# Performance work log

Measured on AMD Instinct MI355X. Metric: run time of the kernel, lower is better.

The kernel has to match this reference:

```python
import jax, jax.numpy as jnp
import numpy as np

MIN_SIZE = 16.0
PH, PW, SCALE = 7, 7, 0.0625


def _context_anchor(rois, hh, hw):
    """rois: [N,5] (batch_idx,x1,y1,x2,y2). Returns [N*8,5] context boxes, col0 = 0 label."""
    N = rois.shape[0]
    x1, y1, x2, y2 = rois[:, 1], rois[:, 2], rois[:, 3], rois[:, 4]
    w, h = x2 - x1, y2 - y1
    k = jnp.arange(3, dtype=rois.dtype)
    sx = x1[:, None] + w[:, None] * (k - 0.5)  # x1 - w + w*k + w/2
    sy = y1[:, None] + h[:, None] * (k - 0.5)
    # np.meshgrid(shift_x, shift_y).ravel() is y-major
    cx = jnp.broadcast_to(sx[:, None, :], (N, 3, 3)).reshape(N, 9)
    cy = jnp.broadcast_to(sy[:, :, None], (N, 3, 3)).reshape(N, 9)
    boxes = jnp.stack([cx - w[:, None] / 4, cy - h[:, None] / 4,
                       cx + w[:, None] / 4, cy + h[:, None] / 4], -1)  # [N,9,4]
    bw = boxes[..., 2] - boxes[..., 0] + 1
    bh = boxes[..., 3] - boxes[..., 1] + 1
    invalid = ((boxes[..., 0] < 0) | (boxes[..., 1] < 0) |
               (boxes[..., 2] >= hw) | (boxes[..., 3] >= hh) |
               (bw < MIN_SIZE) | (bh < MIN_SIZE))
    boxes = jnp.where(invalid[..., None], rois[:, None, 1:5], boxes)
    boxes = boxes[:, jnp.array([0, 1, 2, 3, 5, 6, 7, 8]), :]  # drop center cell
    gt = boxes.reshape(N * 8, 4)  # K = 8N
    # IoU(all roi boxes, gt) with +1 pixel convention (bbox_overlaps_batch)
    A = rois[:, 1:5]
    aw, ah = A[:, 2] - A[:, 0] + 1, A[:, 3] - A[:, 1] + 1
    gw, gh = gt[:, 2] - gt[:, 0] + 1, gt[:, 3] - gt[:, 1] + 1
    iw = jnp.maximum(jnp.minimum(A[:, None, 2], gt[None, :, 2]) - jnp.maximum(A[:, None, 0], gt[None, :, 0]) + 1, 0)
    ih = jnp.maximum(jnp.minimum(A[:, None, 3], gt[None, :, 3]) - jnp.maximum(A[:, None, 1], gt[None, :, 1]) + 1, 0)
    inter = iw * ih
    ov = inter / ((aw * ah)[:, None] + (gw * gh)[None, :] - inter)  # [N,K]
    ov = jnp.where(((gw == 1) & (gh == 1))[None, :], 0.0, ov)
    ov = jnp.where(((aw == 1) & (ah == 1))[:, None], -1.0, ov)
    gt_max = ov.max(0)          # best overlap per gt box
    best = ov.argmax(0)         # index of best-matching roi (torch's `_`)
    labels = gt_max >= 0.3
    w_cell, h_cell = gt[:, 2] - gt[:, 0], gt[:, 3] - gt[:, 1]
    rw = jnp.where(labels, rois[best, 3] - rois[best, 1], 0.0)
    rh = jnp.where(labels, rois[best, 4] - rois[best, 2], 0.0)
    labels = (labels & ~(jnp.maximum(rw, rh) >= jnp.maximum(w_cell, h_cell))
                     & ~(jnp.minimum(rw, rh) < jnp.minimum(w_cell, h_cell) / 3))
    gt = jnp.where(labels[:, None], rois[best][:, 1:5], gt)
    # original zeroes labels at the end -> label column is all zeros
    return jnp.concatenate([jnp.zeros((N * 8, 1), rois.dtype), gt], -1)


def _roi_pool(features, boxes, ph, pw, scale):
    """Classic Caffe max RoIPool. Assumes batch_size==1 (all batch indices 0)."""
    _, C, H, W = features.shape
    f = features[0]  # [C,H,W]
    sw = jnp.round(boxes[:, 1] * scale)
    sh = jnp.round(boxes[:, 2] * scale)
    ew = jnp.round(boxes[:, 3] * scale)
    eh = jnp.round(boxes[:, 4] * scale)
    bsh = jnp.maximum(eh - sh + 1, 1.0) / ph
    bsw = jnp.maximum(ew - sw + 1, 1.0) / pw
    ii = jnp.arange(ph, dtype=f.dtype)
    jj = jnp.arange(pw, dtype=f.dtype)
    hs = jnp.clip(jnp.floor(ii[None, :] * bsh[:, None]) + sh[:, None], 0, H)   # [R,ph]
    he = jnp.clip(jnp.ceil((ii[None, :] + 1) * bsh[:, None]) + sh[:, None], 0, H)
    ws = jnp.clip(jnp.floor(jj[None, :] * bsw[:, None]) + sw[:, None], 0, W)   # [R,pw]
    we = jnp.clip(jnp.ceil((jj[None, :] + 1) * bsw[:, None]) + sw[:, None], 0, W)
    hidx = jnp.arange(H, dtype=f.dtype)
    widx = jnp.arange(W, dtype=f.dtype)
    mask_h = (hidx >= hs[..., None]) & (hidx < he[..., None])  # [R,ph,H]
    mask_w = (widx >= ws[..., None]) & (widx < we[..., None])  # [R,pw,W]
    NEG = jnp.asarray(-1e30, f.dtype)
    # separable masked max: reduce W per pw-bin, then H per ph-bin
    colmax = jnp.stack([jnp.where(mask_w[:, j, None, None, :], f[None], NEG).max(-1)
                        for j in range(pw)], axis=1)           # [R,pw,C,H]
    out = jnp.stack([jnp.where(mask_h[:, i, None, None, :], colmax, NEG).max(-1)
                     for i in range(ph)], axis=1)              # [R,ph,pw,C]
    valid = mask_h.any(-1)[:, :, None] & mask_w.any(-1)[:, None, :]
    out = jnp.where(valid[..., None], out, 0.0)                # empty bins -> 0
    return jnp.transpose(out, (0, 3, 1, 2))                    # [R,C,ph,pw]


def reference(features, rois, hh, hw):
    N = rois.shape[0]
    gt = _context_anchor(rois, hh, hw).reshape(N, 8, 5)
    cat_rois = jnp.concatenate([rois[:, None, :], gt], 1).reshape(-1, 5)  # [9N,5]
    pool = _roi_pool(features, cat_rois, PH, PW, SCALE)                   # [9N,C,7,7]
    pool_feat = pool.reshape(N, -1, PW, PH)                               # [N,9C,7,7]
    return pool_feat, cat_rois


def setup_inputs() -> dict:
    key = jax.random.key(0)
    k1, k2, k3, k4, k5 = jax.random.split(key, 5)
    N, C, Hf, Wf, IMG = 32, 256, 40, 40, 640
    x1 = jax.random.uniform(k1, (N,), minval=0.0, maxval=IMG - 220.0)
    y1 = jax.random.uniform(k2, (N,), minval=0.0, maxval=IMG - 220.0)
    bw = jax.random.uniform(k3, (N,), minval=80.0, maxval=200.0)
    bh = jax.random.uniform(k4, (N,), minval=80.0, maxval=200.0)
    rois = jnp.stack([jnp.zeros((N,)), x1, y1, x1 + bw, y1 + bh], -1).astype(jnp.float32)
    features = jax.random.normal(k5, (1, C, Hf, Wf), dtype=jnp.float32)
    return {"features": features, "rois": rois, "hh": 640, "hw": 640}
```

## Files before the change

### kernel.cpp

```cpp
#include <hip/hip_runtime.h>
#include <math.h>

#define N_ROIS   32
#define N_CAT    (N_ROIS * 9)
#define C_FEAT   256
#define H_FEAT   40
#define W_FEAT   40
#define P_FEAT   (H_FEAT * W_FEAT)
#define PH       7
#define PW       7
#define SCALE    0.0625f
#define MIN_SIZE 16.0f
#define CELLS    (PH * PW)
#define POOL_PER_BOX (C_FEAT * CELLS)
#define OUT_POOL_ELEMS ((size_t)N_CAT * POOL_PER_BOX)

#define CH_G     64
#define NCHG     4
#define NBLK     (N_CAT * NCHG)
#define TPB      448
#define WROWS    14
#define WCOLS    14
#define XSTRIDE  65
#define YSTRIDE  (WROWS * XSTRIDE)
#define WIN_FLTS (WROWS * YSTRIDE + 220)

__global__ __launch_bounds__(TPB) void
fused_v6(const float* __restrict__ f,
         const float* __restrict__ rois,
         const int* __restrict__ hh_p,
         const int* __restrict__ hw_p,
         float* __restrict__ out) {
    __shared__ __align__(16) float win[WIN_FLTS];

    const int bid  = blockIdx.x;
    const int s    = (bid & 7) * (NBLK / 8) + (bid >> 3);
    const int b    = s >> 2;
    const int cg   = s & 3;
    const int tid  = threadIdx.x;
    const int lane = tid & 63;

    const int n  = b / 9;
    const int jj = b % 9;
    const float x1 = rois[n * 5 + 1], y1 = rois[n * 5 + 2];
    const float x2 = rois[n * 5 + 3], y2 = rois[n * 5 + 4];
    float bx1, by1, bx2, by2;

    if (jj == 0) {
        bx1 = x1; by1 = y1; bx2 = x2; by2 = y2;
    } else {
        const int j = jj - 1;
        const int m = (j < 4) ? j : j + 1;
        const int r  = m / 3;
        const int cc = m % 3;
        const float w = x2 - x1, h = y2 - y1;
        const float cx = x1 + w * ((float)cc - 0.5f);
        const float cy = y1 + h * ((float)r  - 0.5f);
        bx1 = cx - w * 0.25f;
        by1 = cy - h * 0.25f;
        bx2 = cx + w * 0.25f;
        by2 = cy + h * 0.25f;
        const float bw = bx2 - bx1 + 1.0f;
        const float bh = by2 - by1 + 1.0f;
        const float hh = (float)(*hh_p);
        const float hw = (float)(*hw_p);
        const bool invalid = (bx1 < 0.0f) || (by1 < 0.0f) ||
                             (bx2 >= hw) || (by2 >= hh) ||
                             (bw < MIN_SIZE) || (bh < MIN_SIZE);
        if (invalid) { bx1 = x1; by1 = y1; bx2 = x2; by2 = y2; }

        const float gw = bx2 - bx1 + 1.0f;
        const float gh = by2 - by1 + 1.0f;
        const float garea = gw * gh;
        const bool gdeg = (gw == 1.0f) && (gh == 1.0f);

        const int a = lane & 31;
        const float ax1 = rois[a * 5 + 1], ay1 = rois[a * 5 + 2];
        const float ax2 = rois[a * 5 + 3], ay2 = rois[a * 5 + 4];
        const float aw = ax2 - ax1 + 1.0f, ah = ay2 - ay1 + 1.0f;
        const float iw = fmaxf(fminf(ax2, bx2) - fmaxf(ax1, bx1) + 1.0f, 0.0f);
        const float ih = fmaxf(fminf(ay2, by2) - fmaxf(ay1, by1) + 1.0f, 0.0f);
        const float inter = iw * ih;
        float ov = inter / (aw * ah + garea - inter);
        if (gdeg) ov = 0.0f;
        if (aw == 1.0f && ah == 1.0f) ov = -1.0f;
        int ai = a;
        #pragma unroll
        for (int off = 32; off >= 1; off >>= 1) {
            const float o2 = __shfl_xor(ov, off);
            const int   a2 = __shfl_xor(ai, off);
            if (o2 > ov || (o2 == ov && a2 < ai)) { ov = o2; ai = a2; }
        }

        bool label = (ov >= 0.3f);
        const float w_cell = bx2 - bx1;
        const float h_cell = by2 - by1;
        const float rw = label ? (rois[ai * 5 + 3] - rois[ai * 5 + 1]) : 0.0f;
        const float rh = label ? (rois[ai * 5 + 4] - rois[ai * 5 + 2]) : 0.0f;
        label = label &&
                !(fmaxf(rw, rh) >= fmaxf(w_cell, h_cell)) &&
                !(fminf(rw, rh) < fminf(w_cell, h_cell) / 3.0f);
        if (label) {
            bx1 = rois[ai * 5 + 1]; by1 = rois[ai * 5 + 2];
            bx2 = rois[ai * 5 + 3]; by2 = rois[ai * 5 + 4];
        }
    }

    if (cg == 0 && tid == 0) {
        float* row = out + OUT_POOL_ELEMS + (size_t)b * 5;
        row[0] = (jj == 0) ? rois[n * 5] : 0.0f;
        row[1] = bx1; row[2] = by1; row[3] = bx2; row[4] = by2;
    }

    const float sw = rintf(bx1 * SCALE);
    const float sh = rintf(by1 * SCALE);
    const float ew = rintf(bx2 * SCALE);
    const float eh = rintf(by2 * SCALE);
    const float bsh = fmaxf(eh - sh + 1.0f, 1.0f) * (1.0f / (float)PH);
    const float bsw = fmaxf(ew - sw + 1.0f, 1.0f) * (1.0f / (float)PW);

    const int cl = tid & 63;
    const int i  = tid >> 6;

    const int hs = __builtin_amdgcn_readfirstlane(
        (int)fminf(fmaxf(floorf((float)i * bsh) + sh, 0.0f), (float)H_FEAT));
    const int he = __builtin_amdgcn_readfirstlane(
        (int)fminf(fmaxf(ceilf((float)(i + 1) * bsh) + sh, 0.0f), (float)H_FEAT));

    int ws[PW], we[PW];
    #pragma unroll
    for (int j = 0; j < PW; ++j) {
        ws[j] = __builtin_amdgcn_readfirstlane(
            (int)fminf(fmaxf(floorf((float)j * bsw) + sw, 0.0f), (float)W_FEAT));
        we[j] = __builtin_amdgcn_readfirstlane(
            (int)fminf(fmaxf(ceilf((float)(j + 1) * bsw) + sw, 0.0f), (float)W_FEAT));
    }
    const int xs = ws[0];
    const int ys = __builtin_amdgcn_readfirstlane(
        (int)fminf(fmaxf(sh, 0.0f), (float)H_FEAT));

    const bool narrow = (bsw <= 2.0f) && (bsh <= 2.0f);

    float mx[PW];
    #pragma unroll
    for (int j = 0; j < PW; ++j) mx[j] = -1e30f;

    if (narrow) {
        {
            const int m  = tid % 7;
            const int ch = tid / 7;
            const int gx0 = (xs + m     < W_FEAT - 1) ? (xs + m)     : (W_FEAT - 1);
            const int gx1 = (xs + m + 7 < W_FEAT - 1) ? (xs + m + 7) : (W_FEAT - 1);
            const float* fch = f + (size_t)(cg * CH_G + ch) * P_FEAT;
            const int l0 = m * XSTRIDE + ch;
            #pragma unroll
            for (int q = 0; q < WROWS; ++q) {
                const int gy = (ys + q < H_FEAT - 1) ? (ys + q) : (H_FEAT - 1);
                const int gb = gy * W_FEAT;
                win[l0 + q * YSTRIDE]               = fch[gb + gx0];
                win[l0 + q * YSTRIDE + 7 * XSTRIDE] = fch[gb + gx1];
            }
        }
        __syncthreads();

        int lo[PW], nj[PW];
        #pragma unroll
        for (int j = 0; j < PW; ++j) {
            lo[j] = ws[j] - xs;
            nj[j] = we[j] - ws[j];
        }
        for (int y = hs; y < he; ++y) {
            const float* wr = win + (y - ys) * YSTRIDE + cl;
            #pragma unroll
            for (int j = 0; j < PW; ++j) {
                const float* p0 = wr + lo[j] * XSTRIDE;
                const float d0 = p0[0];
                const float d1 = p0[XSTRIDE];
                const float d2 = p0[2 * XSTRIDE];
                if (nj[j] > 0) mx[j] = fmaxf(mx[j], d0);
                if (nj[j] > 1) mx[j] = fmaxf(mx[j], d1);
                if (nj[j] > 2) mx[j] = fmaxf(mx[j], d2);
            }
        }
    } else {
        const int c = cg * CH_G + cl;
        for (int y = hs; y < he; ++y) {
            const float* fr = f + (size_t)c * P_FEAT + y * W_FEAT;
            #pragma unroll
            for (int j = 0; j < PW; ++j)
                for (int x = ws[j]; x < we[j]; ++x)
                    mx[j] = fmaxf(mx[j], fr[x]);
        }
    }

    const bool rowv = (he > hs);
    const int c = cg * CH_G + cl;
    float* ob = out + (size_t)b * POOL_PER_BOX + (size_t)c * CELLS + i * PW;
    #pragma unroll
    for (int j = 0; j < PW; ++j)
        ob[j] = (rowv && (we[j] > ws[j])) ? mx[j] : 0.0f;
}

extern "C" void kernel_launch(void* const* d_in, const int* in_sizes, int n_in,
                              void* d_out, int out_size, void* d_ws, size_t ws_size,
                              hipStream_t stream) {
    const float* features = (const float*)d_in[0];
    const float* rois     = (const float*)d_in[1];
    const int*   hh_p     = (const int*)d_in[2];
    const int*   hw_p     = (const int*)d_in[3];

    float* out = (float*)d_out;
    (void)d_ws; (void)ws_size; (void)in_sizes; (void)n_in; (void)out_size;

    hipLaunchKernelGGL(fused_v6, dim3(NBLK), dim3(TPB), 0, stream,
                       features, rois, hh_p, hw_p, out);
}
```

Before: 85.18 us.

## Vectorize window staging with float4 loads and stage output through LDS

Narrow-box staging now loads the feature window as float4 quads along x into a channel-major LDS layout with a padded stride, replacing scalar strided loads. The pooled 64x49 tile is also written back to LDS and then stored to global memory as coalesced float4 writes, instead of each thread writing 7 scattered floats. This is meant to cut global load and store transaction counts, at the cost of extra barriers and possible LDS bank conflicts in the new layout.

```diff
diff --git a/kernel.cpp b/kernel.cpp
--- a/kernel.cpp
+++ b/kernel.cpp
@@ -20,13 +20,16 @@
 #define NBLK     (N_CAT * NCHG)
 #define TPB      448
 #define WROWS    14
-#define WCOLS    14
-#define XSTRIDE  65
-#define YSTRIDE  (WROWS * XSTRIDE)
-#define WIN_FLTS (WROWS * YSTRIDE + 220)
+#define NQ       5
+#define XF       (NQ * 4)
+#define CST      21
+#define YST      (CH_G * CST + 1)
+#define WIN_FLTS (13 * YST + 63 * CST + XF)
+#define OBUF_FLTS (CH_G * CELLS)
+#define STAGE_N  (CH_G * WROWS * NQ)
 
 __global__ __launch_bounds__(TPB) void
-fused_v6(const float* __restrict__ f,
+fused_v7(const float* __restrict__ f,
          const float* __restrict__ rois,
          const int* __restrict__ hh_p,
          const int* __restrict__ hw_p,
@@ -138,52 +141,72 @@
     const int xs = ws[0];
     const int ys = __builtin_amdgcn_readfirstlane(
         (int)fminf(fmaxf(sh, 0.0f), (float)H_FEAT));
+    const int q0 = xs >> 2;
 
     const bool narrow = (bsw <= 2.0f) && (bsh <= 2.0f);
 
-    float mx[PW];
-    #pragma unroll
-    for (int j = 0; j < PW; ++j) mx[j] = -1e30f;
+    const bool rowv = (he > hs);
 
     if (narrow) {
-        {
-            const int m  = tid % 7;
-            const int ch = tid / 7;
-            const int gx0 = (xs + m     < W_FEAT - 1) ? (xs + m)     : (W_FEAT - 1);
-            const int gx1 = (xs + m + 7 < W_FEAT - 1) ? (xs + m + 7) : (W_FEAT - 1);
-            const float* fch = f + (size_t)(cg * CH_G + ch) * P_FEAT;
-            const int l0 = m * XSTRIDE + ch;
-            #pragma unroll
-            for (int q = 0; q < WROWS; ++q) {
-                const int gy = (ys + q < H_FEAT - 1) ? (ys + q) : (H_FEAT - 1);
-                const int gb = gy * W_FEAT;
-                win[l0 + q * YSTRIDE]               = fch[gb + gx0];
-                win[l0 + q * YSTRIDE + 7 * XSTRIDE] = fch[gb + gx1];
-            }
+        const float* fbase = f + (size_t)(cg * CH_G) * P_FEAT;
+        #pragma unroll
+        for (int t = 0; t < STAGE_N / TPB; ++t) {
+            const int e  = tid + t * TPB;
+            const int k  = e % NQ;
+            const int rc = e / NQ;
+            const int yy = rc % WROWS;
+            const int ch = rc / WROWS;
+            const int gy = (ys + yy < H_FEAT - 1) ? (ys + yy) : (H_FEAT - 1);
+            const int gq = (q0 + k < (W_FEAT / 4) - 1) ? (q0 + k) : (W_FEAT / 4) - 1;
+            const float4 v = *(const float4*)(fbase + (size_t)ch * P_FEAT
+                                              + gy * W_FEAT + gq * 4);
+            float* wp = win + yy * YST + ch * CST + k * 4;
+            wp[0] = v.x; wp[1] = v.y; wp[2] = v.z; wp[3] = v.w;
         }
         __syncthreads();
 
-        int lo[PW], nj[PW];
+        float mx[PW];
+        #pragma unroll
+        for (int j = 0; j < PW; ++j) mx[j] = -1e30f;
+
+        int off[PW], nj[PW];
         #pragma unroll
         for (int j = 0; j < PW; ++j) {
-            lo[j] = ws[j] - xs;
-            nj[j] = we[j] - ws[j];
+            off[j] = ws[j] - 4 * q0;
+            nj[j]  = we[j] - ws[j];
         }
         for (int y = hs; y < he; ++y) {
-            const float* wr = win + (y - ys) * YSTRIDE + cl;
+            const float* wr = win + (y - ys) * YST + cl * CST;
             #pragma unroll
             for (int j = 0; j < PW; ++j) {
-                const float* p0 = wr + lo[j] * XSTRIDE;
+                const float* p0 = wr + off[j];
                 const float d0 = p0[0];
-                const float d1 = p0[XSTRIDE];
-                const float d2 = p0[2 * XSTRIDE];
+                const float d1 = p0[1];
+                const float d2 = p0[2];
                 if (nj[j] > 0) mx[j] = fmaxf(mx[j], d0);
                 if (nj[j] > 1) mx[j] = fmaxf(mx[j], d1);
                 if (nj[j] > 2) mx[j] = fmaxf(mx[j], d2);
             }
         }
+        __syncthreads();
+
+        float* orow = win + cl * CELLS + i * PW;
+        #pragma unroll
+        for (int j = 0; j < PW; ++j)
+            orow[j] = (rowv && (nj[j] > 0)) ? mx[j] : 0.0f;
+        __syncthreads();
+
+        const float4* src = (const float4*)win;
+        float4* dst = (float4*)(out + (size_t)b * POOL_PER_BOX
+                                    + (size_t)cg * OBUF_FLTS);
+        dst[tid] = src[tid];
+        const int e2 = tid + TPB;
+        if (e2 < OBUF_FLTS / 4) dst[e2] = src[e2];
     } else {
         const int c = cg * CH_G + cl;
+        float mx[PW];
+        #pragma unroll
+        for (int j = 0; j < PW; ++j) mx[j] = -1e30f;
         for (int y = hs; y < he; ++y) {
             const float* fr = f + (size_t)c * P_FEAT + y * W_FEAT;
             #pragma unroll
@@ -191,14 +214,11 @@
                 for (int x = ws[j]; x < we[j]; ++x)
                     mx[j] = fmaxf(mx[j], fr[x]);
         }
-    }
-
-    const bool rowv = (he > hs);
-    const int c = cg * CH_G + cl;
-    float* ob = out + (size_t)b * POOL_PER_BOX + (size_t)c * CELLS + i * PW;
-    #pragma unroll
-    for (int j = 0; j < PW; ++j)
-        ob[j] = (rowv && (we[j] > ws[j])) ? mx[j] : 0.0f;
+        float* ob = out + (size_t)b * POOL_PER_BOX + (size_t)c * CELLS + i * PW;
+        #pragma unroll
+        for (int j = 0; j < PW; ++j)
+            ob[j] = (rowv && (we[j] > ws[j])) ? mx[j] : 0.0f;
+    }
 }
 
 extern "C" void kernel_launch(void* const* d_in, const int* in_sizes, int n_in,
@@ -212,6 +232,6 @@
     float* out = (float*)d_out;
     (void)d_ws; (void)ws_size; (void)in_sizes; (void)n_in; (void)out_size;
 
-    hipLaunchKernelGGL(fused_v6, dim3(NBLK), dim3(TPB), 0, stream,
+    hipLaunchKernelGGL(fused_v7, dim3(NBLK), dim3(TPB), 0, stream,
                        features, rois, hh_p, hw_p, out);
 }
```

Measured after the change: 78.14 us. 1.09x faster.
